# Performance work log

Measured on AMD Instinct MI355X. Metric: run time of the kernel, lower is better.

## Reference

```python
import jax, jax.numpy as jnp
import numpy as np

B, G, P, E, H, K = 16, 512, 512, 256, 16, 16
CLIP = 10.0

def setup_inputs() -> dict:
    key = jax.random.key(0)
    ks = jax.random.split(key, 10)
    d = {
        "input1": jax.random.normal(ks[0], (B, 1, E), jnp.float32),
        "input2": jax.random.normal(ks[1], (B, G, E), jnp.float32),
        "current_time": jax.random.uniform(ks[2], (B, G, 1), jnp.float32),
        "ninf_mask": jnp.zeros((B, G, P), jnp.float32),
        "encoded_nodes": jax.random.normal(ks[3], (B, P, E), jnp.float32),
        # learned params (Linear weights stored [in, out]; y = x @ W)
        "Wq": jax.random.normal(ks[4], (2 * E + 1, H * K), jnp.float32) / np.sqrt(2 * E + 1),
        "Wk": jax.random.normal(ks[5], (E, H * K), jnp.float32) / np.sqrt(E),
        "Wv": jax.random.normal(ks[6], (E, H * K), jnp.float32) / np.sqrt(E),
        "Wc_w": jax.random.normal(ks[7], (H * K, E), jnp.float32) / np.sqrt(H * K),
        "Wc_b": jax.random.normal(ks[8], (E,), jnp.float32) * 0.01,
    }
    return d

def _heads(x):  # [B, N, H*K] -> [B, H, N, K]
    b, n, _ = x.shape
    return x.reshape(b, n, H, K).transpose(0, 2, 1, 3)

def reference(input1, input2, current_time, ninf_mask, encoded_nodes, Wq, Wk, Wv, Wc_w, Wc_b):
    # reset(): precompute k, v, single_head_key from encoded_nodes
    k = _heads(encoded_nodes @ Wk)  # [B,H,P,K]
    v = _heads(encoded_nodes @ Wv)  # [B,H,P,K]

    # forward()
    input_cat = jnp.concatenate(
        (jnp.broadcast_to(input1, (B, G, E)), input2, current_time), axis=2)  # [B,G,2E+1]
    q = _heads(input_cat @ Wq)  # [B,H,G,K]

    # MHA with additive ninf mask
    score = jnp.einsum("bhgk,bhpk->bhgp", q, k) / np.sqrt(K)
    score = score + ninf_mask[:, None, :, :]
    weights = jax.nn.softmax(score, axis=3)
    out = jnp.einsum("bhgp,bhpk->bhgk", weights, v)
    out_concat = out.transpose(0, 2, 1, 3).reshape(B, G, H * K)
    mh_atten_out = out_concat @ Wc_w + Wc_b  # [B,G,E]

    # single-head pointer score with tanh clipping
    score2 = jnp.einsum("bge,bpe->bgp", mh_atten_out, encoded_nodes) / np.sqrt(E)
    score_clipped = CLIP * jnp.tanh(score2)
    probs = jax.nn.softmax(score_clipped + ninf_mask, axis=2)
    return probs
```

## Files before the change

### kernel.cpp

```cpp
#include <hip/hip_runtime.h>
#include <math.h>

#define BB 16
#define GG 512
#define PP 512
#define EE 256
#define HH 16
#define KD 16
#define HK 256

typedef __bf16 bf16x8 __attribute__((ext_vector_type(8)));
typedef __bf16 bf16x4 __attribute__((ext_vector_type(4)));
typedef float f32x4 __attribute__((ext_vector_type(4)));
typedef float f32x16 __attribute__((ext_vector_type(16)));

#define SA_STRIDE 40
#define SMEM_BYTES 30720

__device__ inline void cvt_split8(const float* __restrict__ p, bf16x8& h, bf16x8& l)
{
    float4 f0 = *(const float4*)p;
    float4 f1 = *(const float4*)(p + 4);
    float v[8] = {f0.x, f0.y, f0.z, f0.w, f1.x, f1.y, f1.z, f1.w};
#pragma unroll
    for (int j = 0; j < 8; ++j) {
        __bf16 hh = (__bf16)v[j];
        h[j] = hh;
        l[j] = (__bf16)(v[j] - (float)hh);
    }
}

__device__ inline void w2proj_body(int bx, int tid, unsigned char* smem,
                                   const float* __restrict__ enc,
                                   const float* __restrict__ Wc,
                                   const float* __restrict__ bias,
                                   __bf16* __restrict__ W2th,
                                   __bf16* __restrict__ W2tl,
                                   float* __restrict__ biasEnc)
{
    __bf16* sAh = (__bf16*)smem;
    __bf16* sAl = sAh + 64 * SA_STRIDE;
    __bf16* sBh = sAl + 64 * SA_STRIDE;
    __bf16* sBl = sBh + 64 * SA_STRIDE;

    const int lane = tid & 63;
    const int w = __builtin_amdgcn_readfirstlane(tid >> 6);
    const int b  = bx >> 5;
    const int t  = bx & 31;
    const int p0 = (t >> 2) * 64;
    const int n0 = (t & 3) * 64;
    const bool do_bias = (n0 == 0);
    const int wm = (w >> 1) * 32, wn = (w & 1) * 32;
    const int ln = lane & 15, kq = (lane >> 4) * 8;
    const int ar = tid >> 2, ac = (tid & 3) * 8;

    f32x4 acc[2][2];
#pragma unroll
    for (int i = 0; i < 2; ++i)
#pragma unroll
        for (int j = 0; j < 2; ++j) acc[i][j] = (f32x4){0.f, 0.f, 0.f, 0.f};
    float bacc = 0.f;

    for (int k0 = 0; k0 < EE; k0 += 32) {
        {
            const float* ap = enc + ((size_t)(b * PP + p0 + ar)) * EE + k0 + ac;
            float4 f0 = *(const float4*)ap;
            float4 f1 = *(const float4*)(ap + 4);
            float v[8] = {f0.x, f0.y, f0.z, f0.w, f1.x, f1.y, f1.z, f1.w};
            bf16x8 h8, l8;
#pragma unroll
            for (int j = 0; j < 8; ++j) {
                __bf16 hh = (__bf16)v[j];
                h8[j] = hh;
                l8[j] = (__bf16)(v[j] - (float)hh);
            }
            if (do_bias) {
#pragma unroll
                for (int j = 0; j < 8; ++j) bacc += v[j] * bias[k0 + ac + j];
            }
            *(bf16x8*)&sAh[ar * SA_STRIDE + ac] = h8;
            *(bf16x8*)&sAl[ar * SA_STRIDE + ac] = l8;
        }
        {
            bf16x8 h8, l8;
            cvt_split8(Wc + (size_t)(n0 + ar) * EE + k0 + ac, h8, l8);
            *(bf16x8*)&sBh[ar * SA_STRIDE + ac] = h8;
            *(bf16x8*)&sBl[ar * SA_STRIDE + ac] = l8;
        }
        __syncthreads();

        bf16x8 ah[2], al[2];
#pragma unroll
        for (int mt = 0; mt < 2; ++mt) {
            ah[mt] = *(const bf16x8*)&sAh[(wm + mt * 16 + ln) * SA_STRIDE + kq];
            al[mt] = *(const bf16x8*)&sAl[(wm + mt * 16 + ln) * SA_STRIDE + kq];
        }
#pragma unroll
        for (int nt = 0; nt < 2; ++nt) {
            const int rowb = wn + nt * 16 + ln;
            bf16x8 bh8 = *(const bf16x8*)&sBh[rowb * SA_STRIDE + kq];
            bf16x8 bl8 = *(const bf16x8*)&sBl[rowb * SA_STRIDE + kq];
#pragma unroll
            for (int mt = 0; mt < 2; ++mt) {
                acc[mt][nt] = __builtin_amdgcn_mfma_f32_16x16x32_bf16(ah[mt], bh8, acc[mt][nt], 0, 0, 0);
                acc[mt][nt] = __builtin_amdgcn_mfma_f32_16x16x32_bf16(al[mt], bh8, acc[mt][nt], 0, 0, 0);
                acc[mt][nt] = __builtin_amdgcn_mfma_f32_16x16x32_bf16(ah[mt], bl8, acc[mt][nt], 0, 0, 0);
            }
        }
        __syncthreads();
    }

    if (do_bias) {
        bacc += __shfl_xor(bacc, 1);
        bacc += __shfl_xor(bacc, 2);
        if ((tid & 3) == 0) biasEnc[b * PP + p0 + ar] = bacc;
    }

    const int rbase = (lane >> 4) * 4;
#pragma unroll
    for (int mt = 0; mt < 2; ++mt)
#pragma unroll
        for (int nt = 0; nt < 2; ++nt)
#pragma unroll
            for (int r = 0; r < 4; ++r) {
                const int p = p0 + wm + mt * 16 + rbase + r;
                const int n = n0 + wn + nt * 16 + ln;
                const float v = acc[mt][nt][r];
                const __bf16 h = (__bf16)v;
                const size_t o = ((size_t)(b * PP + p)) * HK + n;
                W2th[o] = h;
                W2tl[o] = (__bf16)(v - (float)h);
            }
}

__global__ __launch_bounds__(256) void weight_prep(const float* __restrict__ Wk,
                                                   const float* __restrict__ Wv,
                                                   const float* __restrict__ Wq,
                                                   const float* __restrict__ Wc,
                                                   const float* __restrict__ in1,
                                                   const float* __restrict__ enc,
                                                   const float* __restrict__ Wcb,
                                                   __bf16* __restrict__ wkt_h, __bf16* __restrict__ wkt_l,
                                                   __bf16* __restrict__ wvt_h, __bf16* __restrict__ wvt_l,
                                                   __bf16* __restrict__ wqt_h, __bf16* __restrict__ wqt_l,
                                                   float* __restrict__ q1p,
                                                   __bf16* __restrict__ W2th, __bf16* __restrict__ W2tl,
                                                   float* __restrict__ biasEnc)
{
    __shared__ __align__(16) unsigned char smem[4 * 64 * SA_STRIDE * 2];
    if (blockIdx.x < 512) {
        w2proj_body(blockIdx.x, threadIdx.x, smem, enc, Wc, Wcb, W2th, W2tl, biasEnc);
        return;
    }
    int gid = (blockIdx.x - 512) * 256 + threadIdx.x;
    if (gid < 16384) {
        const int b = gid >> 10, q = (gid >> 8) & 3, n = gid & 255;
        const float* ip = in1 + (size_t)b * EE + q * 64;
        const float* wp = Wq + (size_t)(q * 64) * HK + n;
        float acc = 0.f;
#pragma unroll 8
        for (int k = 0; k < 64; ++k) acc += ip[k] * wp[(size_t)k * HK];
        q1p[gid] = acc;
        return;
    }
    int id = gid - 16384;
    if (id >= 196608) return;
    const float* W;
    __bf16 *th, *tl;
    int krow = 0;
    if (id < 65536)       { W = Wk; th = wkt_h; tl = wkt_l; }
    else if (id < 131072) { id -= 65536;  W = Wv; th = wvt_h; tl = wvt_l; }
    else                  { id -= 131072; W = Wq; th = wqt_h; tl = wqt_l; krow = 256; }
    const int k = id & 255;
    const int n = id >> 8;
    const float v = W[(size_t)(k + krow) * HK + n];
    const __bf16 h = (__bf16)v;
    th[(n << 8) + k] = h;
    tl[(n << 8) + k] = (__bf16)(v - (float)h);
}

__device__ inline void kvproj_body(int bx, int tid, unsigned char* smem,
                                   const float* __restrict__ A,
                                   const __bf16* __restrict__ Bkh,
                                   const __bf16* __restrict__ Bkl,
                                   const __bf16* __restrict__ Bvh,
                                   const __bf16* __restrict__ Bvl,
                                   __bf16* __restrict__ Khi,
                                   __bf16* __restrict__ Klo,
                                   __bf16* __restrict__ Vt)
{
    __bf16* sAh = (__bf16*)smem;
    __bf16* sAl = sAh + 64 * SA_STRIDE;
    __bf16* sB  = sAl + 64 * SA_STRIDE;

    const int lane = tid & 63;
    const int w = __builtin_amdgcn_readfirstlane(tid >> 6);
    const int m0 = (bx >> 2) * 64;
    const int n0 = (bx & 3) * 64;
    const int wm = (w >> 1) * 32, wn = (w & 1) * 32;
    const int ln = lane & 15, kq = (lane >> 4) * 8;
    const int ar = tid >> 2, ac = (tid & 3) * 8;

    const __bf16* bsel = (w == 0) ? Bkh : (w == 1) ? Bkl : (w == 2) ? Bvh : Bvl;

    f32x4 ak[2][2], av[2][2];
#pragma unroll
    for (int i = 0; i < 2; ++i)
#pragma unroll
        for (int j = 0; j < 2; ++j) {
            ak[i][j] = (f32x4){0.f, 0.f, 0.f, 0.f};
            av[i][j] = (f32x4){0.f, 0.f, 0.f, 0.f};
        }

    for (int k0 = 0; k0 < EE; k0 += 32) {
        {
            bf16x8 h8, l8;
            cvt_split8(A + (size_t)(m0 + ar) * EE + k0 + ac, h8, l8);
            *(bf16x8*)&sAh[ar * SA_STRIDE + ac] = h8;
            *(bf16x8*)&sAl[ar * SA_STRIDE + ac] = l8;
        }
        {
            const __bf16* src = bsel + (size_t)(n0 + lane) * EE + k0;
            __bf16* dst = sB + (w * 64 + lane) * SA_STRIDE;
            *(bf16x8*)&dst[0]  = *(const bf16x8*)&src[0];
            *(bf16x8*)&dst[8]  = *(const bf16x8*)&src[8];
            *(bf16x8*)&dst[16] = *(const bf16x8*)&src[16];
            *(bf16x8*)&dst[24] = *(const bf16x8*)&src[24];
        }
        __syncthreads();

        bf16x8 ah[2], al[2];
#pragma unroll
        for (int mt = 0; mt < 2; ++mt) {
            ah[mt] = *(const bf16x8*)&sAh[(wm + mt * 16 + ln) * SA_STRIDE + kq];
            al[mt] = *(const bf16x8*)&sAl[(wm + mt * 16 + ln) * SA_STRIDE + kq];
        }
#pragma unroll
        for (int nt = 0; nt < 2; ++nt) {
            const int rowb = wn + nt * 16 + ln;
            bf16x8 bkh8 = *(const bf16x8*)&sB[(0 * 64 + rowb) * SA_STRIDE + kq];
            bf16x8 bkl8 = *(const bf16x8*)&sB[(1 * 64 + rowb) * SA_STRIDE + kq];
            bf16x8 bvh8 = *(const bf16x8*)&sB[(2 * 64 + rowb) * SA_STRIDE + kq];
            bf16x8 bvl8 = *(const bf16x8*)&sB[(3 * 64 + rowb) * SA_STRIDE + kq];
#pragma unroll
            for (int mt = 0; mt < 2; ++mt) {
                ak[mt][nt] = __builtin_amdgcn_mfma_f32_16x16x32_bf16(ah[mt], bkh8, ak[mt][nt], 0, 0, 0);
                ak[mt][nt] = __builtin_amdgcn_mfma_f32_16x16x32_bf16(al[mt], bkh8, ak[mt][nt], 0, 0, 0);
                ak[mt][nt] = __builtin_amdgcn_mfma_f32_16x16x32_bf16(ah[mt], bkl8, ak[mt][nt], 0, 0, 0);
                av[mt][nt] = __builtin_amdgcn_mfma_f32_16x16x32_bf16(ah[mt], bvh8, av[mt][nt], 0, 0, 0);
                av[mt][nt] = __builtin_amdgcn_mfma_f32_16x16x32_bf16(al[mt], bvh8, av[mt][nt], 0, 0, 0);
                av[mt][nt] = __builtin_amdgcn_mfma_f32_16x16x32_bf16(ah[mt], bvl8, av[mt][nt], 0, 0, 0);
            }
        }
        __syncthreads();
    }

    __bf16* eKh = (__bf16*)smem;
    __bf16* eKl = eKh + 5120;
    __bf16* eV  = eKl + 5120;

    const int rbase = (lane >> 4) * 4;
#pragma unroll
    for (int mt = 0; mt < 2; ++mt)
#pragma unroll
        for (int nt = 0; nt < 2; ++nt) {
            const int hloc = (w & 1) * 2 + nt;
            const int nl = wn + nt * 16 + ln;
#pragma unroll
            for (int r = 0; r < 4; ++r) {
                const int m = wm + mt * 16 + rbase + r;
                const float vk = ak[mt][nt][r];
                const __bf16 hk = (__bf16)vk;
                eKh[(hloc * 64 + m) * 20 + ln] = hk;
                eKl[(hloc * 64 + m) * 20 + ln] = (__bf16)(vk - (float)hk);
                eV[nl * 68 + m] = (__bf16)av[mt][nt][r];
            }
        }
    __syncthreads();

    const int b = m0 >> 9;
    const int pbase = m0 & (PP - 1);
    {
        const int hl = tid >> 6, p = tid & 63;
        const int hg = (n0 >> 4) + hl;
        const size_t dst = (((size_t)b * HH + hg) * PP + pbase + p) * KD;
        const int base = (hl * 64 + p) * 20;
        uint2 a0 = *(const uint2*)&eKh[base + 0];
        uint2 a1 = *(const uint2*)&eKh[base + 4];
        uint2 a2 = *(const uint2*)&eKh[base + 8];
        uint2 a3 = *(const uint2*)&eKh[base + 12];
        *(uint4*)(Khi + dst)     = make_uint4(a0.x, a0.y, a1.x, a1.y);
        *(uint4*)(Khi + dst + 8) = make_uint4(a2.x, a2.y, a3.x, a3.y);
        uint2 c0 = *(const uint2*)&eKl[base + 0];
        uint2 c1 = *(const uint2*)&eKl[base + 4];
        uint2 c2 = *(const uint2*)&eKl[base + 8];
        uint2 c3 = *(const uint2*)&eKl[base + 12];
        *(uint4*)(Klo + dst)     = make_uint4(c0.x, c0.y, c1.x, c1.y);
        *(uint4*)(Klo + dst + 8) = make_uint4(c2.x, c2.y, c3.x, c3.y);
    }
    {
        const int n = tid >> 2, qq = tid & 3;
        const int ng = n0 + n, hg = ng >> 4, kk = ng & 15;
        const int base = n * 68 + qq * 16;
        uint2 v0 = *(const uint2*)&eV[base + 0];
        uint2 v1 = *(const uint2*)&eV[base + 4];
        uint2 v2 = *(const uint2*)&eV[base + 8];
        uint2 v3 = *(const uint2*)&eV[base + 12];
        const size_t dst = ((((size_t)b * HH + hg) * KD + kk) * PP) + pbase + qq * 16;
        *(uint4*)(Vt + dst)     = make_uint4(v0.x, v0.y, v1.x, v1.y);
        *(uint4*)(Vt + dst + 8) = make_uint4(v2.x, v2.y, v3.x, v3.y);
    }
}

__device__ inline void qproj_body(int bx, int tid, unsigned char* smem,
                                  const float* __restrict__ in2,
                                  const float* __restrict__ ct,
                                  const __bf16* __restrict__ Bh,
                                  const __bf16* __restrict__ Bl,
                                  const float* __restrict__ WqFull,
                                  const float* __restrict__ q1p,
                                  __bf16* __restrict__ Qhi,
                                  __bf16* __restrict__ Qlo)
{
    __bf16* sAh = (__bf16*)smem;
    __bf16* sAl = sAh + 64 * SA_STRIDE;
    __bf16* sB  = sAl + 64 * SA_STRIDE;

    const int lane = tid & 63;
    const int w = __builtin_amdgcn_readfirstlane(tid >> 6);
    const int m0 = (bx >> 2) * 64;
    const int n0 = (bx & 3) * 64;
    const int wm = (w >> 1) * 32, wn = (w & 1) * 32;
    const int ln = lane & 15, kq = (lane >> 4) * 8;
    const int ar = tid >> 2, ac = (tid & 3) * 8;
    const int b = m0 >> 9;
    const float* WqLast = WqFull + (size_t)512 * HK;

    f32x4 acc[2][2];
#pragma unroll
    for (int i = 0; i < 2; ++i)
#pragma unroll
        for (int j = 0; j < 2; ++j) acc[i][j] = (f32x4){0.f, 0.f, 0.f, 0.f};

    for (int k0 = 0; k0 < EE; k0 += 32) {
        {
            bf16x8 h8, l8;
            cvt_split8(in2 + (size_t)(m0 + ar) * EE + k0 + ac, h8, l8);
            *(bf16x8*)&sAh[ar * SA_STRIDE + ac] = h8;
            *(bf16x8*)&sAl[ar * SA_STRIDE + ac] = l8;
        }
        {
            const int mat = w >> 1;
            const int row = (w & 1) * 32 + (lane >> 1);
            const int half = (lane & 1) * 16;
            const __bf16* src = (mat ? Bl : Bh) + ((size_t)(n0 + row) << 8) + k0 + half;
            __bf16* dst = sB + (mat * 64 + row) * SA_STRIDE + half;
            *(bf16x8*)&dst[0] = *(const bf16x8*)&src[0];
            *(bf16x8*)&dst[8] = *(const bf16x8*)&src[8];
        }
        __syncthreads();

        bf16x8 ah[2], al[2];
#pragma unroll
        for (int mt = 0; mt < 2; ++mt) {
            ah[mt] = *(const bf16x8*)&sAh[(wm + mt * 16 + ln) * SA_STRIDE + kq];
            al[mt] = *(const bf16x8*)&sAl[(wm + mt * 16 + ln) * SA_STRIDE + kq];
        }
#pragma unroll
        for (int nt = 0; nt < 2; ++nt) {
            const int rowb = wn + nt * 16 + ln;
            bf16x8 bh8 = *(const bf16x8*)&sB[(0 * 64 + rowb) * SA_STRIDE + kq];
            bf16x8 bl8 = *(const bf16x8*)&sB[(1 * 64 + rowb) * SA_STRIDE + kq];
#pragma unroll
            for (int mt = 0; mt < 2; ++mt) {
                acc[mt][nt] = __builtin_amdgcn_mfma_f32_16x16x32_bf16(ah[mt], bh8, acc[mt][nt], 0, 0, 0);
                acc[mt][nt] = __builtin_amdgcn_mfma_f32_16x16x32_bf16(al[mt], bh8, acc[mt][nt], 0, 0, 0);
                acc[mt][nt] = __builtin_amdgcn_mfma_f32_16x16x32_bf16(ah[mt], bl8, acc[mt][nt], 0, 0, 0);
            }
        }
        __syncthreads();
    }

    __bf16* eQh = (__bf16*)smem;
    __bf16* eQl = eQh + 5120;

    const int rbase = (lane >> 4) * 4;
#pragma unroll
    for (int mt = 0; mt < 2; ++mt)
#pragma unroll
        for (int nt = 0; nt < 2; ++nt) {
            const int hloc = (w & 1) * 2 + nt;
            const int ng = n0 + wn + nt * 16 + ln;
            const float wq = WqLast[ng];
            const float q1v = q1p[b * 1024 + 0 * 256 + ng] + q1p[b * 1024 + 1 * 256 + ng]
                            + q1p[b * 1024 + 2 * 256 + ng] + q1p[b * 1024 + 3 * 256 + ng];
#pragma unroll
            for (int r = 0; r < 4; ++r) {
                const int m = wm + mt * 16 + rbase + r;
                const float v = acc[mt][nt][r] + q1v + ct[m0 + m] * wq;
                const __bf16 h = (__bf16)v;
                eQh[(hloc * 64 + m) * 20 + ln] = h;
                eQl[(hloc * 64 + m) * 20 + ln] = (__bf16)(v - (float)h);
            }
        }
    __syncthreads();

    {
        const int hl = tid >> 6, p = tid & 63;
        const int hg = (n0 >> 4) + hl;
        const int g = (m0 & (GG - 1)) + p;
        const size_t dst = (((size_t)b * HH + hg) * GG + g) * KD;
        const int base = (hl * 64 + p) * 20;
        uint2 a0 = *(const uint2*)&eQh[base + 0];
        uint2 a1 = *(const uint2*)&eQh[base + 4];
        uint2 a2 = *(const uint2*)&eQh[base + 8];
        uint2 a3 = *(const uint2*)&eQh[base + 12];
        *(uint4*)(Qhi + dst)     = make_uint4(a0.x, a0.y, a1.x, a1.y);
        *(uint4*)(Qhi + dst + 8) = make_uint4(a2.x, a2.y, a3.x, a3.y);
        uint2 c0 = *(const uint2*)&eQl[base + 0];
        uint2 c1 = *(const uint2*)&eQl[base + 4];
        uint2 c2 = *(const uint2*)&eQl[base + 8];
        uint2 c3 = *(const uint2*)&eQl[base + 12];
        *(uint4*)(Qlo + dst)     = make_uint4(c0.x, c0.y, c1.x, c1.y);
        *(uint4*)(Qlo + dst + 8) = make_uint4(c2.x, c2.y, c3.x, c3.y);
    }
}

__global__ __launch_bounds__(256, 2) void fused_proj(const float* __restrict__ enc,
                                                     const __bf16* __restrict__ Bkh,
                                                     const __bf16* __restrict__ Bkl,
                                                     const __bf16* __restrict__ Bvh,
                                                     const __bf16* __restrict__ Bvl,
                                                     __bf16* __restrict__ Khi,
                                                     __bf16* __restrict__ Klo,
                                                     __bf16* __restrict__ Vt,
                                                     const float* __restrict__ in2,
                                                     const float* __restrict__ ct,
                                                     const __bf16* __restrict__ Bqh,
                                                     const __bf16* __restrict__ Bql,
                                                     const float* __restrict__ WqFull,
                                                     const float* __restrict__ q1p,
                                                     __bf16* __restrict__ Qhi,
                                                     __bf16* __restrict__ Qlo)
{
    __shared__ __align__(16) unsigned char smem[SMEM_BYTES];
    const int id = blockIdx.x;
    if (id < 512)
        kvproj_body(id, threadIdx.x, smem, enc, Bkh, Bkl, Bvh, Bvl, Khi, Klo, Vt);
    else
        qproj_body(id - 512, threadIdx.x, smem, in2, ct, Bqh, Bql, WqFull, q1p, Qhi, Qlo);
}

#define AT_STRIDE 264

__global__ __launch_bounds__(1024, 4) void attn_ptr(const __bf16* __restrict__ Qhi,
                                                    const __bf16* __restrict__ Qlo,
                                                    const __bf16* __restrict__ Khi,
                                                    const __bf16* __restrict__ Klo,
                                                    const __bf16* __restrict__ Vt,
                                                    const __bf16* __restrict__ w2_hi,
                                                    const __bf16* __restrict__ w2_lo,
                                                    const float* __restrict__ biasEnc,
                                                    const float* __restrict__ mask,
                                                    float* __restrict__ out)
{
    __shared__ __align__(16) float smask[32][512];
    __shared__ __align__(16) __bf16 sP[16][32][40];
    __shared__ float srs[16][32];
    __shared__ __align__(16) __bf16 sAth[32][AT_STRIDE];
    __shared__ __align__(16) __bf16 sAtl[32][AT_STRIDE];

    const int t = threadIdx.x;
    const int lane = t & 63;
    const int w = __builtin_amdgcn_readfirstlane(t >> 6);
    const int id = blockIdx.x;
    const int b = id & 15;
    const int g0 = (id >> 4) * 32;
    const int ln32 = lane & 31;
    const int half = lane >> 5;
    const int ln16 = lane & 15;
    const int quad = (lane >> 4) & 3;
    const int h = w;

    {
        const float* msrc = mask + ((size_t)(b * GG + g0)) * PP;
        float* smf = &smask[0][0];
#pragma unroll
        for (int i = 0; i < 4; ++i) {
            const int idx = (t + i * 1024) * 4;
            *(float4*)&smf[idx] = *(const float4*)&msrc[idx];
        }
    }
    __syncthreads();

    const size_t qbase = (((size_t)b * HH + h) * GG + g0) * KD;
    const size_t kbase = ((size_t)b * HH + h) * PP * KD;
    const size_t vbase = ((size_t)b * HH + h) * KD * PP;

    bf16x8 qah = *(const bf16x8*)(Qhi + qbase + (size_t)ln32 * KD + half * 8);
    bf16x8 qal = *(const bf16x8*)(Qlo + qbase + (size_t)ln32 * KD + half * 8);

    float rs[16];
#pragma unroll
    for (int r = 0; r < 16; ++r) rs[r] = 0.f;
    f32x4 o0 = (f32x4){0.f, 0.f, 0.f, 0.f};
    f32x4 o1 = (f32x4){0.f, 0.f, 0.f, 0.f};

#pragma unroll 2
    for (int pc = 0; pc < 16; ++pc) {
        const int pb = pc * 32;
        const size_t ko = kbase + (size_t)(pb + ln32) * KD + half * 8;
        bf16x8 kh = *(const bf16x8*)(Khi + ko);
        bf16x8 kl = *(const bf16x8*)(Klo + ko);
        bf16x8 vb = *(const bf16x8*)(Vt + vbase + (size_t)ln16 * PP + pb + quad * 8);

        f32x16 s = (f32x16){0.f, 0.f, 0.f, 0.f, 0.f, 0.f, 0.f, 0.f,
                            0.f, 0.f, 0.f, 0.f, 0.f, 0.f, 0.f, 0.f};
        __builtin_amdgcn_s_setprio(1);
        s = __builtin_amdgcn_mfma_f32_32x32x16_bf16(qah, kh, s, 0, 0, 0);
        s = __builtin_amdgcn_mfma_f32_32x32x16_bf16(qal, kh, s, 0, 0, 0);
        s = __builtin_amdgcn_mfma_f32_32x32x16_bf16(qah, kl, s, 0, 0, 0);
        __builtin_amdgcn_s_setprio(0);

#pragma unroll
        for (int r = 0; r < 16; ++r) {
            const int row = (r & 3) + 8 * (r >> 2) + 4 * half;
            const float m = smask[row][pb + ln32];
            const float e = __expf(s[r] * 0.25f + m);
            rs[r] += e;
            sP[w][row][ln32] = (__bf16)e;
        }

        bf16x8 p0 = *(const bf16x8*)&sP[w][ln16][quad * 8];
        bf16x8 p1 = *(const bf16x8*)&sP[w][16 + ln16][quad * 8];
        __builtin_amdgcn_s_setprio(1);
        o0 = __builtin_amdgcn_mfma_f32_16x16x32_bf16(p0, vb, o0, 0, 0, 0);
        o1 = __builtin_amdgcn_mfma_f32_16x16x32_bf16(p1, vb, o1, 0, 0, 0);
        __builtin_amdgcn_s_setprio(0);
    }

#pragma unroll
    for (int r = 0; r < 16; ++r) {
#pragma unroll
        for (int mm = 1; mm < 32; mm <<= 1) rs[r] += __shfl_xor(rs[r], mm);
    }
    if (ln32 == 0) {
#pragma unroll
        for (int r = 0; r < 16; ++r)
            srs[w][(r & 3) + 8 * (r >> 2) + 4 * half] = rs[r];
    }

#pragma unroll
    for (int t2 = 0; t2 < 2; ++t2) {
        const f32x4 oc = t2 ? o1 : o0;
#pragma unroll
        for (int r = 0; r < 4; ++r) {
            const int grow = t2 * 16 + quad * 4 + r;
            const float v = oc[r] / srs[w][grow];
            const __bf16 hv = (__bf16)v;
            sAth[grow][w * 16 + ln16] = hv;
            sAtl[grow][w * 16 + ln16] = (__bf16)(v - (float)hv);
        }
    }
    __syncthreads();

    const size_t brow = ((size_t)(b * PP + w * 32 + ln32)) * HK + half * 8;
    const float be = biasEnc[b * PP + w * 32 + ln32];

    f32x16 acc0 = (f32x16){0.f, 0.f, 0.f, 0.f, 0.f, 0.f, 0.f, 0.f,
                           0.f, 0.f, 0.f, 0.f, 0.f, 0.f, 0.f, 0.f};
    f32x16 acc1 = acc0, acc2 = acc0;

#pragma unroll 4
    for (int kc = 0; kc < HK; kc += 16) {
        bf16x8 ah = *(const bf16x8*)&sAth[ln32][kc + half * 8];
        bf16x8 al = *(const bf16x8*)&sAtl[ln32][kc + half * 8];
        bf16x8 bh = *(const bf16x8*)(w2_hi + brow + kc);
        bf16x8 bl = *(const bf16x8*)(w2_lo + brow + kc);
        __builtin_amdgcn_s_setprio(1);
        acc0 = __builtin_amdgcn_mfma_f32_32x32x16_bf16(ah, bh, acc0, 0, 0, 0);
        acc1 = __builtin_amdgcn_mfma_f32_32x32x16_bf16(al, bh, acc1, 0, 0, 0);
        acc2 = __builtin_amdgcn_mfma_f32_32x32x16_bf16(ah, bl, acc2, 0, 0, 0);
        __builtin_amdgcn_s_setprio(0);
    }

    f32x16 acc = acc0 + acc1 + acc2;

    float rsum[16];
#pragma unroll
    for (int r = 0; r < 16; ++r) {
        const int row = (r & 3) + 8 * (r >> 2) + 4 * half;
        float s = (acc[r] + be) * 0.0625f;
        s = fminf(9.f, fmaxf(-9.f, s));
        const float e2 = __expf(2.f * s);
        const float th = (e2 - 1.f) / (e2 + 1.f);
        const float m = smask[row][w * 32 + ln32];
        const float e = __expf(10.f * th + m);
        acc[r] = e;
        rsum[r] = e;
    }

#pragma unroll
    for (int r = 0; r < 16; ++r) {
        rsum[r] += __shfl_xor(rsum[r], 1);
        rsum[r] += __shfl_xor(rsum[r], 2);
        rsum[r] += __shfl_xor(rsum[r], 4);
        rsum[r] += __shfl_xor(rsum[r], 8);
        rsum[r] += __shfl_xor(rsum[r], 16);
    }
    if (ln32 == 0) {
#pragma unroll
        for (int r = 0; r < 16; ++r)
            srs[w][(r & 3) + 8 * (r >> 2) + 4 * half] = rsum[r];
    }
    __syncthreads();

    float inv[16];
#pragma unroll
    for (int r = 0; r < 16; ++r) {
        const int row = (r & 3) + 8 * (r >> 2) + 4 * half;
        float tot = 0.f;
#pragma unroll
        for (int wv = 0; wv < 16; ++wv) tot += srs[wv][row];
        inv[r] = 1.f / tot;
    }

#pragma unroll
    for (int r = 0; r < 16; ++r) {
        const int row = (r & 3) + 8 * (r >> 2) + 4 * half;
        out[((size_t)(b * GG + g0 + row)) * PP + w * 32 + ln32] = acc[r] * inv[r];
    }
}

extern "C" void kernel_launch(void* const* d_in, const int* in_sizes, int n_in,
                              void* d_out, int out_size, void* d_ws, size_t ws_size,
                              hipStream_t stream)
{
    const float* in1  = (const float*)d_in[0];
    const float* in2  = (const float*)d_in[1];
    const float* ct   = (const float*)d_in[2];
    const float* mask = (const float*)d_in[3];
    const float* enc  = (const float*)d_in[4];
    const float* Wq   = (const float*)d_in[5];
    const float* Wk   = (const float*)d_in[6];
    const float* Wv   = (const float*)d_in[7];
    const float* Wcw  = (const float*)d_in[8];
    const float* Wcb  = (const float*)d_in[9];
    float* out = (float*)d_out;
    float* ws  = (float*)d_ws;

    const size_t SEG = (size_t)BB * GG * HK;
    __bf16* Khi = (__bf16*)ws;
    __bf16* Klo = Khi + SEG;
    __bf16* Vt  = (__bf16*)(ws + SEG);
    __bf16* Qhi = (__bf16*)(ws + 2 * SEG);
    __bf16* Qlo = Qhi + SEG;
    __bf16* wkt_h = (__bf16*)(ws + 3 * SEG);
    __bf16* wkt_l = wkt_h + 65536;
    __bf16* wvt_h = wkt_l + 65536;
    __bf16* wvt_l = wvt_h + 65536;
    __bf16* wqt_h = wvt_l + 65536;
    __bf16* wqt_l = wqt_h + 65536;
    float*  q1p     = ws + 3 * SEG + 196608;
    float*  biasEnc = q1p + 16384;
    __bf16* W2th  = (__bf16*)(ws + 4 * SEG);
    __bf16* W2tl  = W2th + SEG;

    const dim3 blk(256);

    weight_prep<<<dim3(1344), blk, 0, stream>>>(Wk, Wv, Wq, Wcw, in1, enc, Wcb,
                                                wkt_h, wkt_l, wvt_h, wvt_l,
                                                wqt_h, wqt_l, q1p,
                                                W2th, W2tl, biasEnc);

    fused_proj<<<dim3(1024), blk, 0, stream>>>(enc, wkt_h, wkt_l, wvt_h, wvt_l,
                                               Khi, Klo, Vt,
                                               in2, ct, wqt_h, wqt_l, Wq, q1p,
                                               Qhi, Qlo);

    attn_ptr<<<dim3(256), dim3(1024), 0, stream>>>(Qhi, Qlo, Khi, Klo, Vt,
                                                   W2th, W2tl, biasEnc, mask, out);
}
```

Measured before the change: 177.1 us.

## Keep attention probabilities in registers via transposed score MFMA and lane shuffles

The score MFMA now computes the transposed product (K×Q), so each lane owns one query row and can read its mask slice with vector LDS loads. The per-wave LDS staging buffer for probabilities is removed. Probabilities are packed to bf16 with v_cvt_pk_bf16 and exchanged across wave halves with shuffles to form the PV operand directly, using 32x32x16 MFMAs over the V tile. The row sum reduces to a single scalar per lane, and the mask buffer is padded to cut bank conflicts. In exchange the code relies on exact MFMA register layouts and needs extra cross-lane shuffles.

New measurement: 174.7 us. Within noise of the previous version (-1.3%).

```diff
diff --git a/kernel.cpp b/kernel.cpp
--- a/kernel.cpp
+++ b/kernel.cpp
@@ -13,6 +13,7 @@
 typedef __bf16 bf16x4 __attribute__((ext_vector_type(4)));
 typedef float f32x4 __attribute__((ext_vector_type(4)));
 typedef float f32x16 __attribute__((ext_vector_type(16)));
+typedef int i32x4 __attribute__((ext_vector_type(4)));
 
 #define SA_STRIDE 40
 #define SMEM_BYTES 30720
@@ -28,6 +29,13 @@
         h[j] = hh;
         l[j] = (__bf16)(v[j] - (float)hh);
     }
+}
+
+__device__ inline int cvt_pk_bf16(float lo, float hi)
+{
+    int r;
+    asm("v_cvt_pk_bf16_f32 %0, %1, %2" : "=v"(r) : "v"(lo), "v"(hi));
+    return r;
 }
 
 __device__ inline void w2proj_body(int bx, int tid, unsigned char* smem,
@@ -452,6 +460,7 @@
 }
 
 #define AT_STRIDE 264
+#define MSK_STRIDE 516
 
 __global__ __launch_bounds__(1024, 4) void attn_ptr(const __bf16* __restrict__ Qhi,
                                                     const __bf16* __restrict__ Qlo,
@@ -464,8 +473,7 @@
                                                     const float* __restrict__ mask,
                                                     float* __restrict__ out)
 {
-    __shared__ __align__(16) float smask[32][512];
-    __shared__ __align__(16) __bf16 sP[16][32][40];
+    __shared__ __align__(16) float smask[32][MSK_STRIDE];
     __shared__ float srs[16][32];
     __shared__ __align__(16) __bf16 sAth[32][AT_STRIDE];
     __shared__ __align__(16) __bf16 sAtl[32][AT_STRIDE];
@@ -478,17 +486,15 @@
     const int g0 = (id >> 4) * 32;
     const int ln32 = lane & 31;
     const int half = lane >> 5;
-    const int ln16 = lane & 15;
-    const int quad = (lane >> 4) & 3;
     const int h = w;
 
     {
         const float* msrc = mask + ((size_t)(b * GG + g0)) * PP;
-        float* smf = &smask[0][0];
 #pragma unroll
         for (int i = 0; i < 4; ++i) {
-            const int idx = (t + i * 1024) * 4;
-            *(float4*)&smf[idx] = *(const float4*)&msrc[idx];
+            const int c = (t + i * 1024) * 4;
+            const int row = c >> 9, col = c & 511;
+            *(float4*)&smask[row][col] = *(const float4*)&msrc[row * 512 + col];
         }
     }
     __syncthreads();
@@ -500,11 +506,10 @@
     bf16x8 qah = *(const bf16x8*)(Qhi + qbase + (size_t)ln32 * KD + half * 8);
     bf16x8 qal = *(const bf16x8*)(Qlo + qbase + (size_t)ln32 * KD + half * 8);
 
-    float rs[16];
-#pragma unroll
-    for (int r = 0; r < 16; ++r) rs[r] = 0.f;
-    f32x4 o0 = (f32x4){0.f, 0.f, 0.f, 0.f};
-    f32x4 o1 = (f32x4){0.f, 0.f, 0.f, 0.f};
+    float rs = 0.f;
+    f32x16 acc = (f32x16){0.f, 0.f, 0.f, 0.f, 0.f, 0.f, 0.f, 0.f,
+                          0.f, 0.f, 0.f, 0.f, 0.f, 0.f, 0.f, 0.f};
+    const int dv = ln32 & 15;
 
 #pragma unroll 2
     for (int pc = 0; pc < 16; ++pc) {
@@ -512,58 +517,84 @@
         const size_t ko = kbase + (size_t)(pb + ln32) * KD + half * 8;
         bf16x8 kh = *(const bf16x8*)(Khi + ko);
         bf16x8 kl = *(const bf16x8*)(Klo + ko);
-        bf16x8 vb = *(const bf16x8*)(Vt + vbase + (size_t)ln16 * PP + pb + quad * 8);
+        bf16x8 vb0 = *(const bf16x8*)(Vt + vbase + (size_t)dv * PP + pb + half * 8);
+        bf16x8 vb1 = *(const bf16x8*)(Vt + vbase + (size_t)dv * PP + pb + 16 + half * 8);
 
         f32x16 s = (f32x16){0.f, 0.f, 0.f, 0.f, 0.f, 0.f, 0.f, 0.f,
                             0.f, 0.f, 0.f, 0.f, 0.f, 0.f, 0.f, 0.f};
         __builtin_amdgcn_s_setprio(1);
-        s = __builtin_amdgcn_mfma_f32_32x32x16_bf16(qah, kh, s, 0, 0, 0);
-        s = __builtin_amdgcn_mfma_f32_32x32x16_bf16(qal, kh, s, 0, 0, 0);
-        s = __builtin_amdgcn_mfma_f32_32x32x16_bf16(qah, kl, s, 0, 0, 0);
+        s = __builtin_amdgcn_mfma_f32_32x32x16_bf16(kh, qah, s, 0, 0, 0);
+        s = __builtin_amdgcn_mfma_f32_32x32x16_bf16(kh, qal, s, 0, 0, 0);
+        s = __builtin_amdgcn_mfma_f32_32x32x16_bf16(kl, qah, s, 0, 0, 0);
         __builtin_amdgcn_s_setprio(0);
 
+        const float4 m0 = *(const float4*)&smask[ln32][pb + 0  + 4 * half];
+        const float4 m1 = *(const float4*)&smask[ln32][pb + 8  + 4 * half];
+        const float4 m2 = *(const float4*)&smask[ln32][pb + 16 + 4 * half];
+        const float4 m3 = *(const float4*)&smask[ln32][pb + 24 + 4 * half];
+        s[0]  = __expf(s[0]  * 0.25f + m0.x);
+        s[1]  = __expf(s[1]  * 0.25f + m0.y);
+        s[2]  = __expf(s[2]  * 0.25f + m0.z);
+        s[3]  = __expf(s[3]  * 0.25f + m0.w);
+        s[4]  = __expf(s[4]  * 0.25f + m1.x);
+        s[5]  = __expf(s[5]  * 0.25f + m1.y);
+        s[6]  = __expf(s[6]  * 0.25f + m1.z);
+        s[7]  = __expf(s[7]  * 0.25f + m1.w);
+        s[8]  = __expf(s[8]  * 0.25f + m2.x);
+        s[9]  = __expf(s[9]  * 0.25f + m2.y);
+        s[10] = __expf(s[10] * 0.25f + m2.z);
+        s[11] = __expf(s[11] * 0.25f + m2.w);
+        s[12] = __expf(s[12] * 0.25f + m3.x);
+        s[13] = __expf(s[13] * 0.25f + m3.y);
+        s[14] = __expf(s[14] * 0.25f + m3.z);
+        s[15] = __expf(s[15] * 0.25f + m3.w);
+#pragma unroll
+        for (int r = 0; r < 16; ++r) rs += s[r];
+
+        const int w01 = cvt_pk_bf16(s[0],  s[1]);
+        const int w23 = cvt_pk_bf16(s[2],  s[3]);
+        const int w45 = cvt_pk_bf16(s[4],  s[5]);
+        const int w67 = cvt_pk_bf16(s[6],  s[7]);
+        const int w89 = cvt_pk_bf16(s[8],  s[9]);
+        const int wAB = cvt_pk_bf16(s[10], s[11]);
+        const int wCD = cvt_pk_bf16(s[12], s[13]);
+        const int wEF = cvt_pk_bf16(s[14], s[15]);
+        const int x1 = half ? w01 : w45;
+        const int x2 = half ? w23 : w67;
+        const int x3 = half ? w89 : wCD;
+        const int x4 = half ? wAB : wEF;
+        const int p1 = __shfl_xor(x1, 32);
+        const int p2 = __shfl_xor(x2, 32);
+        const int p3 = __shfl_xor(x3, 32);
+        const int p4 = __shfl_xor(x4, 32);
+        i32x4 f0 = half ? (i32x4){p1, p2, w45, w67} : (i32x4){w01, w23, p1, p2};
+        i32x4 f1 = half ? (i32x4){p3, p4, wCD, wEF} : (i32x4){w89, wAB, p3, p4};
+        bf16x8 pa0 = *(bf16x8*)&f0;
+        bf16x8 pa1 = *(bf16x8*)&f1;
+
+        __builtin_amdgcn_s_setprio(1);
+        acc = __builtin_amdgcn_mfma_f32_32x32x16_bf16(pa0, vb0, acc, 0, 0, 0);
+        acc = __builtin_amdgcn_mfma_f32_32x32x16_bf16(pa1, vb1, acc, 0, 0, 0);
+        __builtin_amdgcn_s_setprio(0);
+    }
+
+    rs += __shfl_xor(rs, 32);
+    if (half == 0) srs[w][ln32] = rs;
+
+    if (ln32 < 16) {
 #pragma unroll
         for (int r = 0; r < 16; ++r) {
-            const int row = (r & 3) + 8 * (r >> 2) + 4 * half;
-            const float m = smask[row][pb + ln32];
-            const float e = __expf(s[r] * 0.25f + m);
-            rs[r] += e;
-            sP[w][row][ln32] = (__bf16)e;
-        }
-
-        bf16x8 p0 = *(const bf16x8*)&sP[w][ln16][quad * 8];
-        bf16x8 p1 = *(const bf16x8*)&sP[w][16 + ln16][quad * 8];
-        __builtin_amdgcn_s_setprio(1);
-        o0 = __builtin_amdgcn_mfma_f32_16x16x32_bf16(p0, vb, o0, 0, 0, 0);
-        o1 = __builtin_amdgcn_mfma_f32_16x16x32_bf16(p1, vb, o1, 0, 0, 0);
-        __builtin_amdgcn_s_setprio(0);
-    }
-
-#pragma unroll
-    for (int r = 0; r < 16; ++r) {
-#pragma unroll
-        for (int mm = 1; mm < 32; mm <<= 1) rs[r] += __shfl_xor(rs[r], mm);
-    }
-    if (ln32 == 0) {
-#pragma unroll
-        for (int r = 0; r < 16; ++r)
-            srs[w][(r & 3) + 8 * (r >> 2) + 4 * half] = rs[r];
-    }
-
-#pragma unroll
-    for (int t2 = 0; t2 < 2; ++t2) {
-        const f32x4 oc = t2 ? o1 : o0;
-#pragma unroll
-        for (int r = 0; r < 4; ++r) {
-            const int grow = t2 * 16 + quad * 4 + r;
-            const float v = oc[r] / srs[w][grow];
+            const int g = (r & 3) + 8 * (r >> 2) + 4 * half;
+            const float v = acc[r] / srs[w][g];
             const __bf16 hv = (__bf16)v;
-            sAth[grow][w * 16 + ln16] = hv;
-            sAtl[grow][w * 16 + ln16] = (__bf16)(v - (float)hv);
+            sAth[g][w * 16 + ln32] = hv;
+            sAtl[g][w * 16 + ln32] = (__bf16)(v - (float)hv);
         }
     }
     __syncthreads();
 
+    const int ln16 = lane & 15;
+    (void)ln16;
     const size_t brow = ((size_t)(b * PP + w * 32 + ln32)) * HK + half * 8;
     const float be = biasEnc[b * PP + w * 32 + ln32];
 
@@ -584,19 +615,19 @@
         __builtin_amdgcn_s_setprio(0);
     }
 
-    f32x16 acc = acc0 + acc1 + acc2;
+    f32x16 pacc = acc0 + acc1 + acc2;
 
     float rsum[16];
 #pragma unroll
     for (int r = 0; r < 16; ++r) {
         const int row = (r & 3) + 8 * (r >> 2) + 4 * half;
-        float s = (acc[r] + be) * 0.0625f;
-        s = fminf(9.f, fmaxf(-9.f, s));
-        const float e2 = __expf(2.f * s);
+        float sc = (pacc[r] + be) * 0.0625f;
+        sc = fminf(9.f, fmaxf(-9.f, sc));
+        const float e2 = __expf(2.f * sc);
         const float th = (e2 - 1.f) / (e2 + 1.f);
         const float m = smask[row][w * 32 + ln32];
         const float e = __expf(10.f * th + m);
-        acc[r] = e;
+        pacc[r] = e;
         rsum[r] = e;
     }
 
@@ -628,7 +659,7 @@
 #pragma unroll
     for (int r = 0; r < 16; ++r) {
         const int row = (r & 3) + 8 * (r >> 2) + 4 * half;
-        out[((size_t)(b * GG + g0 + row)) * PP + w * 32 + ln32] = acc[r] * inv[r];
+        out[((size_t)(b * GG + g0 + row)) * PP + w * 32 + ln32] = pacc[r] * inv[r];
     }
 }
 
```
